# Performance work log

Measured on AMD Instinct MI355X. Metric: run time of the kernel, lower is better.

The kernel has to match this reference:

```python
import jax, jax.numpy as jnp
import numpy as np

PI = 3.1415926
EPS_LN = 1e-5
SLOPE = 0.01  # nn.LeakyReLU default negative_slope


def _leaky(x):
    return jnp.where(x >= 0, x, SLOPE * x)


def _layernorm(x):
    # normalizes over dims (1,2) of [B,C,L], biased variance
    mean = x.mean(axis=(1, 2), keepdims=True)
    var = x.var(axis=(1, 2), keepdims=True)
    return (x - mean) / jnp.sqrt(var + EPS_LN)


def _conv1d(x, w, b):
    # x [B,C,L], w [O,I,3]
    y = jax.lax.conv_general_dilated(x, w, window_strides=(1,), padding='SAME',
                                     dimension_numbers=('NCH', 'OIH', 'NCH'))
    return y + b[None, :, None]


def _conv_stack(x, w1, b1, w2, b2, w3, b3):
    x = _leaky(_layernorm(_conv1d(x, w1, b1)))
    x = _leaky(_layernorm(_conv1d(x, w2, b2)))
    x = _leaky(_layernorm(_conv1d(x, w3, b3)))
    return x


def _context_pooling(feats, w1, b1, w2, b2, w3, b3, r=0.1):
    # feats [B,L,D]
    B, L, D = feats.shape
    sw = _conv_stack(feats.transpose(0, 2, 1), w1, b1, w2, b2, w3, b3)  # [B,2,L]
    s = jax.nn.softmax(sw[:, 0, :], axis=1)  # [B,L]
    w = jax.nn.softmax(sw[:, 1, :], axis=1)  # [B,L]
    std = r * L * s  # [B,L] (per query/center i)
    pos = jnp.arange(L, dtype=feats.dtype)
    diff2 = (pos[None, :] - pos[:, None]) ** 2  # [Li,Lj], (place - center)^2
    g = (2 * PI) ** -0.5 * (std[:, :, None] ** -1) * jnp.exp(
        -diff2[None] / (1e-5 + 2.0 * std[:, :, None] ** 2))  # [B,Li,Lj]
    g = g / jnp.max(g, axis=2, keepdims=True)
    W = g * w[:, None, :]  # [B,Li,Lj]
    return jnp.einsum('bij,bjd->bid', W, feats)


def setup_inputs() -> dict:
    key = jax.random.key(0)
    ks = jax.random.split(key, 16)
    B, L, D = 16, 1024, 640
    D2 = 2 * D
    f32 = jnp.float32
    sc = 0.02
    inp = {
        'feats': jax.random.normal(ks[0], (B, L, D), f32),
        # ContextPooling conv stack
        'cp_w1': jax.random.normal(ks[1], (D2, D, 3), f32) * sc,
        'cp_b1': jnp.zeros((D2,), f32),
        'cp_w2': jax.random.normal(ks[2], (D2, D2, 3), f32) * sc,
        'cp_b2': jnp.zeros((D2,), f32),
        'cp_w3': jax.random.normal(ks[3], (2, D2, 3), f32) * sc,
        'cp_b3': jnp.zeros((2,), f32),
        # SoluModel conv stack
        'cv_w1': jax.random.normal(ks[4], (D2, D, 3), f32) * sc,
        'cv_b1': jnp.zeros((D2,), f32),
        'cv_w2': jax.random.normal(ks[5], (D2, D2, 3), f32) * sc,
        'cv_b2': jnp.zeros((D2,), f32),
        'cv_w3': jax.random.normal(ks[6], (D, D2, 3), f32) * sc,
        'cv_b3': jnp.zeros((D,), f32),
        # MLP: Linear(2D -> D), torch init normal(0, 0.01), bias 0
        'mlp_w': jax.random.normal(ks[7], (D, 2 * D), f32) * 0.01,
        'mlp_b': jnp.zeros((D,), f32),
    }
    return inp


def reference(feats, cp_w1, cp_b1, cp_w2, cp_b2, cp_w3, cp_b3,
              cv_w1, cv_b1, cv_w2, cv_b2, cv_w3, cv_b3, mlp_w, mlp_b):
    out_sa = _context_pooling(feats, cp_w1, cp_b1, cp_w2, cp_b2, cp_w3, cp_b3) + feats
    out_conv = _conv_stack(feats.transpose(0, 2, 1),
                           cv_w1, cv_b1, cv_w2, cv_b2, cv_w3, cv_b3)
    out_conv = out_conv.transpose(0, 2, 1) + feats
    out = jnp.concatenate([out_sa, out_conv], axis=2)  # [B,L,2D]
    # Dropout(p=0.6) is identity at inference
    out = _leaky(jnp.einsum('bld,od->blo', out, mlp_w) + mlp_b)
    return out
```

## Files before the change

kernel.cpp:

```cpp
#include <hip/hip_runtime.h>
#include <hip/hip_bf16.h>
#include <math.h>

#define SLOPE 0.01f
#define EPS_LN 1e-5f

typedef __hip_bfloat16 bf16;
typedef __attribute__((ext_vector_type(8))) short short8;
typedef __attribute__((ext_vector_type(4))) float f32x4;

__device__ __forceinline__ float leakyf(float x) { return x < 0.f ? SLOPE * x : x; }

__device__ __forceinline__ float b2f(short s) {
    unsigned u = ((unsigned)(unsigned short)s) << 16;
    return __builtin_bit_cast(float, u);
}
__device__ __forceinline__ short f2b(float f) {
    __hip_bfloat16 h = __float2bfloat16(f);
    return *(short*)&h;
}

__device__ __forceinline__ void gload_lds16(const void* g, void* l) {
    __builtin_amdgcn_global_load_lds(
        (const __attribute__((address_space(1))) void*)g,
        (__attribute__((address_space(3))) void*)l, 16, 0, 0);
}

template <int EPI>
__global__ __launch_bounds__(256, 2) void gemm_dual(
    const bf16* __restrict__ A0, const bf16* __restrict__ A1, long sA, int ldA,
    const bf16* __restrict__ Bt0, const bf16* __restrict__ Bt1,
    const float* __restrict__ bias0, const float* __restrict__ bias1,
    void* __restrict__ Out0, void* __restrict__ Out1, long sO, int ldO, int K,
    int gx, int gy, int halfwg,
    float2* __restrict__ stats0, float2* __restrict__ stats1)
{
    __shared__ bf16 As[128][64];
    __shared__ bf16 Bs[128][64];

    const int nwg = gridDim.x;
    const int wid = (blockIdx.x & 7) * (nwg >> 3) + (blockIdx.x >> 3);
    const int branch = wid >= halfwg;
    const int w = wid - branch * halfwg;
    const int bx = w % gx;
    const int by = (w / gx) % gy;
    const int bz = w / (gx * gy);

    const bf16* A = branch ? A1 : A0;
    const bf16* Bt = branch ? Bt1 : Bt0;
    const float* bias = branch ? bias1 : bias0;
    void* Outv = branch ? Out1 : Out0;
    float2* stats = branch ? stats1 : stats0;

    const bf16* Ab = A + (long)bz * sA + (long)by * 128 * ldA;
    const bf16* Bb = Bt + (long)bx * 128 * K;
    const int tid = threadIdx.x;
    const int wave = tid >> 6, lane = tid & 63;
    const int moff = (wave >> 1) * 64, noff = (wave & 1) * 64;
    const int r16 = lane & 15, g4 = lane >> 4;
    const int r7 = r16 & 7;

    f32x4 acc[4][4];
#pragma unroll
    for (int i = 0; i < 4; ++i)
#pragma unroll
        for (int j = 0; j < 4; ++j)
            acc[i][j] = (f32x4){0.f, 0.f, 0.f, 0.f};

    for (int k0 = 0; k0 < K; k0 += 64) {
        __syncthreads();
#pragma unroll
        for (int i = 0; i < 4; ++i) {
            int chunk = i * 256 + tid;
            int row = chunk >> 3;
            int kc = (chunk ^ (chunk >> 3)) & 7;
            gload_lds16(Ab + (long)row * ldA + (k0 + kc * 8),
                        (char*)(&As[0][0]) + (i * 256 + wave * 64) * 16);
        }
#pragma unroll
        for (int i = 0; i < 4; ++i) {
            int chunk = i * 256 + tid;
            int row = chunk >> 3;
            int kc = (chunk ^ (chunk >> 3)) & 7;
            gload_lds16(Bb + (long)row * K + (k0 + kc * 8),
                        (char*)(&Bs[0][0]) + (i * 256 + wave * 64) * 16);
        }
        __syncthreads();
#pragma unroll
        for (int kk = 0; kk < 2; ++kk) {
            short8 af[4], bfr[4];
#pragma unroll
            for (int mi = 0; mi < 4; ++mi)
                af[mi] = *(const short8*)&As[moff + mi * 16 + r16][((kk * 4 + g4) ^ r7) * 8];
#pragma unroll
            for (int ni = 0; ni < 4; ++ni)
                bfr[ni] = *(const short8*)&Bs[noff + ni * 16 + r16][((kk * 4 + g4) ^ r7) * 8];
#pragma unroll
            for (int mi = 0; mi < 4; ++mi)
#pragma unroll
                for (int ni = 0; ni < 4; ++ni)
                    acc[mi][ni] = __builtin_amdgcn_mfma_f32_16x16x32_bf16(
                        af[mi], bfr[ni], acc[mi][ni], 0, 0, 0);
        }
    }

    float s = 0.f, q = 0.f;
#pragma unroll
    for (int mi = 0; mi < 4; ++mi) {
#pragma unroll
        for (int ni = 0; ni < 4; ++ni) {
            int col = bx * 128 + noff + ni * 16 + r16;
            float bv = bias[col];
#pragma unroll
            for (int r = 0; r < 4; ++r) {
                int row = by * 128 + moff + mi * 16 + g4 * 4 + r;
                float v = acc[mi][ni][r] + bv;
                if (EPI == 1) {
                    ((float*)Outv)[(long)bz * sO + (long)row * ldO + col] = leakyf(v);
                } else {
                    ((bf16*)Outv)[(long)bz * sO + (long)row * ldO + col] = __float2bfloat16(v);
                    s += v; q += v * v;
                }
            }
        }
    }
    if (EPI == 0) {
        __syncthreads();
        float* red = (float*)&As[0][0];
        float* red2 = red + 256;
        red[tid] = s; red2[tid] = q;
        __syncthreads();
        for (int o = 128; o; o >>= 1) {
            if (tid < o) { red[tid] += red[tid + o]; red2[tid] += red2[tid + o]; }
            __syncthreads();
        }
        if (tid == 0) {
            atomicAdd(&stats[bz].x, red[0]);
            atomicAdd(&stats[bz].y, red2[0]);
        }
    }
}

__device__ __forceinline__ void repack1(const float* __restrict__ w,
                                        bf16* __restrict__ bt, long idx, int CI)
{
    int K3 = 3 * CI;
    int o = (int)(idx / K3);
    int k = (int)(idx % K3);
    int t = k / CI, ci = k % CI;
    bt[idx] = __float2bfloat16(w[(long)o * CI * 3 + ci * 3 + t]);
}

__global__ void prep_k(const float* __restrict__ feats,
                       const float* __restrict__ cp_w1, const float* __restrict__ cv_w1,
                       const float* __restrict__ cp_w2, const float* __restrict__ cv_w2,
                       const float* __restrict__ cp_w3, const float* __restrict__ cv_w3,
                       const float* __restrict__ mlp_w,
                       bf16* __restrict__ xp,
                       bf16* __restrict__ Bm1a, bf16* __restrict__ Bm1b,
                       bf16* __restrict__ Bcp2, bf16* __restrict__ Bcv2,
                       bf16* __restrict__ Bcp3, bf16* __restrict__ Bcv3,
                       bf16* __restrict__ Bmlp, float2* __restrict__ sacc)
{
    long idx = (long)blockIdx.x * 256 + threadIdx.x;
    if (idx < 80) { sacc[idx] = make_float2(0.f, 0.f); return; }
    idx -= 80;
    const long NPACK8 = 16L * 1026 * 640 / 8;
    if (idx < NPACK8) {
        long e = idx * 8;
        int c = (int)(e % 640);
        long t = e / 640;
        int r = (int)(t % 1026);
        int b = (int)(t / 1026);
        short8 o;
        if (r == 0 || r == 1025) {
#pragma unroll
            for (int j = 0; j < 8; ++j) o[j] = 0;
        } else {
            const float* src = feats + ((long)b * 1024 + (r - 1)) * 640 + c;
            f32x4 v0 = *(const f32x4*)src;
            f32x4 v1 = *(const f32x4*)(src + 4);
#pragma unroll
            for (int j = 0; j < 4; ++j) { o[j] = f2b(v0[j]); o[j + 4] = f2b(v1[j]); }
        }
        *(short8*)(xp + e) = o;
        return;
    }
    idx -= NPACK8;
    const long W1 = 1280L * 640 * 3;
    const long W2 = 1280L * 1280 * 3;
    if (idx < W1) { repack1(cp_w1, Bm1a, idx, 640); return; }
    idx -= W1;
    if (idx < W1) { repack1(cv_w1, Bm1b, idx, 640); return; }
    idx -= W1;
    if (idx < W2) { repack1(cp_w2, Bcp2, idx, 1280); return; }
    idx -= W2;
    if (idx < W2) { repack1(cv_w2, Bcv2, idx, 1280); return; }
    idx -= W2;
    if (idx < 2L * 1280 * 3) { repack1(cp_w3, Bcp3, idx, 1280); return; }
    idx -= 2L * 1280 * 3;
    const long W3 = 640L * 1280 * 3;
    if (idx < W3) { repack1(cv_w3, Bcv3, idx, 1280); return; }
    idx -= W3;
    if (idx < 640L * 1280) { Bmlp[idx] = __float2bfloat16(mlp_w[idx]); return; }
}

__global__ void norm_pack2_k(const bf16* __restrict__ y0, const bf16* __restrict__ y1,
                             bf16* __restrict__ x0, bf16* __restrict__ x1,
                             const float2* __restrict__ sacc, int sbase, float invN)
{
    const int prob = blockIdx.y;
    const bf16* y = prob ? y1 : y0;
    bf16* xp = prob ? x1 : x0;
    long i8 = (long)blockIdx.x * 256 + threadIdx.x;
    const long total8 = 16L * 1026 * 1280 / 8;
    if (i8 >= total8) return;
    long e = i8 * 8;
    int c = (int)(e % 1280);
    long t = e / 1280;
    int r = (int)(t % 1026);
    int b = (int)(t / 1026);
    short8 o;
    if (r == 0 || r == 1025) {
#pragma unroll
        for (int j = 0; j < 8; ++j) o[j] = 0;
    } else {
        float2 a = sacc[sbase + prob * 16 + b];
        float m = a.x * invN;
        float rstd = rsqrtf(a.y * invN - m * m + EPS_LN);
        short8 v = *(const short8*)(y + ((long)b * 1024 + (r - 1)) * 1280 + c);
#pragma unroll
        for (int j = 0; j < 8; ++j)
            o[j] = f2b(leakyf((b2f(v[j]) - m) * rstd));
    }
    *(short8*)(xp + e) = o;
}

__global__ void norm_addf_v_k(const bf16* __restrict__ y, const float2* __restrict__ sacc,
                              const float* __restrict__ feats, bf16* __restrict__ acat,
                              float invN)
{
    long i8 = (long)blockIdx.x * 256 + threadIdx.x;
    long total8 = 16L * 1024 * 640 / 8;
    if (i8 >= total8) return;
    long e = i8 * 8;
    int c = (int)(e % 640);
    int l = (int)((e / 640) % 1024);
    int b = (int)(e / (640L * 1024));
    float2 a = sacc[64 + b];
    float m = a.x * invN;
    float rstd = rsqrtf(a.y * invN - m * m + EPS_LN);
    short8 v = *(const short8*)(y + e);
    f32x4 f0 = *(const f32x4*)(feats + e);
    f32x4 f1 = *(const f32x4*)(feats + e + 4);
    short8 o;
#pragma unroll
    for (int j = 0; j < 4; ++j) {
        o[j] = f2b(leakyf((b2f(v[j]) - m) * rstd) + f0[j]);
        o[j + 4] = f2b(leakyf((b2f(v[j + 4]) - m) * rstd) + f1[j]);
    }
    *(short8*)(acat + ((long)b * 1024 + l) * 1280 + 640 + c) = o;
}

__global__ void conv3cp_k(const bf16* __restrict__ xp, const bf16* __restrict__ w3,
                          const float* __restrict__ b3, float* __restrict__ sw)
{
    int wid = (int)((blockIdx.x * 256 + threadIdx.x) >> 6);
    int lane = threadIdx.x & 63;
    int b = wid >> 10, l = wid & 1023;
    const short8* xr = (const short8*)(xp + ((long)b * 1026 + l) * 1280);
    const short8* w0 = (const short8*)w3;
    const short8* w1 = (const short8*)(w3 + 3840);
    float a0 = 0.f, a1 = 0.f;
    for (int c = lane; c < 480; c += 64) {
        short8 x = xr[c], u = w0[c], v = w1[c];
#pragma unroll
        for (int j = 0; j < 8; ++j) {
            float xf = b2f(x[j]);
            a0 += xf * b2f(u[j]);
            a1 += xf * b2f(v[j]);
        }
    }
    for (int o = 32; o; o >>= 1) { a0 += __shfl_down(a0, o); a1 += __shfl_down(a1, o); }
    if (lane == 0) {
        sw[b * 2048 + l] = a0 + b3[0];
        sw[b * 2048 + 1024 + l] = a1 + b3[1];
    }
}

__global__ __launch_bounds__(256) void cp_post_k(const float* __restrict__ sw,
                                                 float* __restrict__ stdb,
                                                 float* __restrict__ wb)
{
    int b = blockIdx.x, tid = threadIdx.x;
    __shared__ float s0[1024], s1[1024], red[256];
    const float* p = sw + b * 2048;
    float s = 0.f, q = 0.f;
    for (int l = tid; l < 1024; l += 256) {
        float v0 = p[l], v1 = p[1024 + l];
        s0[l] = v0; s1[l] = v1;
        s += v0 + v1; q += v0 * v0 + v1 * v1;
    }
    red[tid] = s; __syncthreads();
    for (int o = 128; o; o >>= 1) { if (tid < o) red[tid] += red[tid + o]; __syncthreads(); }
    float mean = red[0] / 2048.f; __syncthreads();
    red[tid] = q; __syncthreads();
    for (int o = 128; o; o >>= 1) { if (tid < o) red[tid] += red[tid + o]; __syncthreads(); }
    float inv = rsqrtf(red[0] / 2048.f - mean * mean + EPS_LN); __syncthreads();
    for (int l = tid; l < 1024; l += 256) {
        s0[l] = leakyf((s0[l] - mean) * inv);
        s1[l] = leakyf((s1[l] - mean) * inv);
    }
    __syncthreads();
    float mx = -1e30f;
    for (int l = tid; l < 1024; l += 256) mx = fmaxf(mx, s0[l]);
    red[tid] = mx; __syncthreads();
    for (int o = 128; o; o >>= 1) { if (tid < o) red[tid] = fmaxf(red[tid], red[tid + o]); __syncthreads(); }
    mx = red[0]; __syncthreads();
    float se = 0.f;
    for (int l = tid; l < 1024; l += 256) { float e = __expf(s0[l] - mx); s0[l] = e; se += e; }
    red[tid] = se; __syncthreads();
    for (int o = 128; o; o >>= 1) { if (tid < o) red[tid] += red[tid + o]; __syncthreads(); }
    float rs = 1.f / red[0]; __syncthreads();
    for (int l = tid; l < 1024; l += 256) stdb[b * 1024 + l] = 102.4f * s0[l] * rs;
    mx = -1e30f;
    for (int l = tid; l < 1024; l += 256) mx = fmaxf(mx, s1[l]);
    red[tid] = mx; __syncthreads();
    for (int o = 128; o; o >>= 1) { if (tid < o) red[tid] = fmaxf(red[tid], red[tid + o]); __syncthreads(); }
    mx = red[0]; __syncthreads();
    se = 0.f;
    for (int l = tid; l < 1024; l += 256) { float e = __expf(s1[l] - mx); s1[l] = e; se += e; }
    red[tid] = se; __syncthreads();
    for (int o = 128; o; o >>= 1) { if (tid < o) red[tid] += red[tid + o]; __syncthreads(); }
    rs = 1.f / red[0]; __syncthreads();
    for (int l = tid; l < 1024; l += 256) wb[b * 1024 + l] = s1[l] * rs;
}

__global__ __launch_bounds__(256) void pool_k(const float* __restrict__ feats,
                                              const float* __restrict__ stdb,
                                              const float* __restrict__ wb,
                                              bf16* __restrict__ acat)
{
    int i = blockIdx.x, b = blockIdx.y, tid = threadIdx.x;
    float sd = stdb[b * 1024 + i];
    float den = 1e-5f + 2.f * sd * sd;
    float inv = 1.f / den;
    int R = (int)sqrtf(11.5129255f * den) + 1;
    int jlo = max(0, i - R), jhi = min(1023, i + R);
    __shared__ float cj[256];
    float a0 = 0.f, a1 = 0.f, a2 = 0.f;
    const float* fb = feats + (long)b * 1024 * 640;
    for (int j0 = jlo; j0 <= jhi; j0 += 256) {
        int j = j0 + tid;
        float c = 0.f;
        if (j <= jhi) {
            float d = (float)(j - i);
            c = __expf(-d * d * inv) * wb[b * 1024 + j];
        }
        __syncthreads();
        cj[tid] = c;
        __syncthreads();
        int lim = min(256, jhi - j0 + 1);
        for (int t = 0; t < lim; ++t) {
            float cc = cj[t];
            const float* fr = fb + (long)(j0 + t) * 640;
            a0 += cc * fr[tid];
            a1 += cc * fr[tid + 256];
            if (tid < 128) a2 += cc * fr[tid + 512];
        }
    }
    long obase = ((long)b * 1024 + i) * 1280;
    long fbase = ((long)b * 1024 + i) * 640;
    acat[obase + tid] = __float2bfloat16(a0 + feats[fbase + tid]);
    acat[obase + tid + 256] = __float2bfloat16(a1 + feats[fbase + tid + 256]);
    if (tid < 128) acat[obase + tid + 512] = __float2bfloat16(a2 + feats[fbase + tid + 512]);
}

extern "C" void kernel_launch(void* const* d_in, const int* in_sizes, int n_in,
                              void* d_out, int out_size, void* d_ws, size_t ws_size,
                              hipStream_t stream)
{
    const float* feats = (const float*)d_in[0];
    const float* cp_w1 = (const float*)d_in[1];
    const float* cp_b1 = (const float*)d_in[2];
    const float* cp_w2 = (const float*)d_in[3];
    const float* cp_b2 = (const float*)d_in[4];
    const float* cp_w3 = (const float*)d_in[5];
    const float* cp_b3 = (const float*)d_in[6];
    const float* cv_w1 = (const float*)d_in[7];
    const float* cv_b1 = (const float*)d_in[8];
    const float* cv_w2 = (const float*)d_in[9];
    const float* cv_b2 = (const float*)d_in[10];
    const float* cv_w3 = (const float*)d_in[11];
    const float* cv_b3 = (const float*)d_in[12];
    const float* mlp_w = (const float*)d_in[13];
    const float* mlp_b = (const float*)d_in[14];
    float* out = (float*)d_out;

    char* ws = (char*)d_ws;
    size_t off = 0;
    auto alloc = [&](size_t bytes) -> char* {
        char* p = ws + off;
        off += (bytes + 255) & ~(size_t)255;
        return p;
    };
    char* R1 = alloc(16L * 1024 * 1280 * 2);
    bf16* XpadF = (bf16*)R1;
    bf16* Acat = (bf16*)R1;
    bf16* Xp_cp = (bf16*)alloc(16L * 1026 * 1280 * 2);
    bf16* Xp_cv = (bf16*)alloc(16L * 1026 * 1280 * 2);
    bf16* Y0 = (bf16*)alloc(16L * 1024 * 1280 * 2);
    bf16* Y1 = (bf16*)alloc(16L * 1024 * 1280 * 2);
    bf16* Ycv3 = Y0;
    bf16* Bm1 = (bf16*)alloc(2560L * 1920 * 2);
    bf16* Bcp2 = (bf16*)alloc(1280L * 3840 * 2);
    bf16* Bcv2 = (bf16*)alloc(1280L * 3840 * 2);
    bf16* Bcp3 = (bf16*)alloc(2L * 3840 * 2);
    bf16* Bcv3 = (bf16*)alloc(640L * 3840 * 2);
    bf16* Bmlp = (bf16*)alloc(640L * 1280 * 2);
    float* swb = (float*)alloc(16L * 2048 * 4);
    float* stdb = (float*)alloc(16L * 1024 * 4);
    float* wbf = (float*)alloc(16L * 1024 * 4);
    float2* sacc = (float2*)alloc(80L * 8);
    (void)ws_size; (void)in_sizes; (void)n_in; (void)out_size;

    const long N28 = 16L * 1026 * 1280 / 8;
    const long NA8 = 16L * 1024 * 640 / 8;
    const long N1280 = 1024L * 1280, N640 = 1024L * 640;
    const float inv1280 = 1.f / (float)N1280, inv640 = 1.f / (float)N640;

    const long NPREP = 80 + 16L * 1026 * 640 / 8 + 2 * (1280L * 640 * 3)
                     + 2 * (1280L * 1280 * 3) + 2L * 1280 * 3
                     + 640L * 1280 * 3 + 640L * 1280;
    prep_k<<<(int)((NPREP + 255) / 256), 256, 0, stream>>>(
        feats, cp_w1, cv_w1, cp_w2, cv_w2, cp_w3, cv_w3, mlp_w,
        XpadF, Bm1, Bm1 + 1280L * 1920, Bcp2, Bcv2, Bcp3, Bcv3, Bmlp, sacc);

    gemm_dual<0><<<2560, 256, 0, stream>>>(
        XpadF, XpadF, 1026L * 640, 640, Bm1, Bm1 + 1280L * 1920,
        cp_b1, cv_b1, Y0, Y1, N1280, 1280, 1920, 10, 8, 1280,
        sacc, sacc + 16);
    norm_pack2_k<<<dim3((N28 + 255) / 256, 2), 256, 0, stream>>>(
        Y0, Y1, Xp_cp, Xp_cv, sacc, 0, inv1280);

    gemm_dual<0><<<2560, 256, 0, stream>>>(
        Xp_cp, Xp_cv, 1026L * 1280, 1280, Bcp2, Bcv2,
        cp_b2, cv_b2, Y0, Y1, N1280, 1280, 3840, 10, 8, 1280,
        sacc + 32, sacc + 48);
    norm_pack2_k<<<dim3((N28 + 255) / 256, 2), 256, 0, stream>>>(
        Y0, Y1, Xp_cp, Xp_cv, sacc, 32, inv1280);

    conv3cp_k<<<4096, 256, 0, stream>>>(Xp_cp, Bcp3, cp_b3, swb);
    cp_post_k<<<16, 256, 0, stream>>>(swb, stdb, wbf);
    pool_k<<<dim3(1024, 16), 256, 0, stream>>>(feats, stdb, wbf, Acat);

    gemm_dual<0><<<640, 256, 0, stream>>>(
        Xp_cv, Xp_cv, 1026L * 1280, 1280, Bcv3, Bcv3,
        cv_b3, cv_b3, Ycv3, Ycv3, N640, 640, 3840, 5, 8, 640,
        sacc + 64, sacc + 64);
    norm_addf_v_k<<<(NA8 + 255) / 256, 256, 0, stream>>>(Ycv3, sacc, feats, Acat, inv640);

    gemm_dual<1><<<640, 256, 0, stream>>>(
        Acat, Acat, N1280, 1280, Bmlp, Bmlp,
        mlp_b, mlp_b, out, out, N640, 640, 1280, 5, 8, 640,
        nullptr, nullptr);
}
```

Measured before the change: 738.1 us.

## Fuse cv3 GEMM and context pooling into one heterogeneous launch with 4-query pool blocks

```diff
diff --git a/kernel.cpp b/kernel.cpp
--- a/kernel.cpp
+++ b/kernel.cpp
@@ -137,6 +137,158 @@
         if (tid == 0) {
             atomicAdd(&stats[bz].x, red[0]);
             atomicAdd(&stats[bz].y, red2[0]);
+        }
+    }
+}
+
+__global__ __launch_bounds__(256, 2) void cv3_pool_k(
+    const bf16* __restrict__ Axp, const bf16* __restrict__ Bt,
+    const float* __restrict__ bias, bf16* __restrict__ Y,
+    float2* __restrict__ stats,
+    const float* __restrict__ feats, const float* __restrict__ stdb,
+    const float* __restrict__ wb, bf16* __restrict__ acat)
+{
+    __shared__ bf16 As[128][64];
+    __shared__ bf16 Bs[128][64];
+    __shared__ float cj4[4][256];
+
+    const int tid = threadIdx.x;
+    if (blockIdx.x < 640) {
+        const int wid = (blockIdx.x & 7) * 80 + (blockIdx.x >> 3);
+        const int bx = wid % 5;
+        const int by = (wid / 5) % 8;
+        const int bz = wid / 40;
+        const int K = 3840;
+        const bf16* Ab = Axp + ((long)bz * 1026 + (long)by * 128) * 1280;
+        const bf16* Bb = Bt + (long)bx * 128 * K;
+        const int wave = tid >> 6, lane = tid & 63;
+        const int moff = (wave >> 1) * 64, noff = (wave & 1) * 64;
+        const int r16 = lane & 15, g4 = lane >> 4;
+        const int r7 = r16 & 7;
+
+        f32x4 acc[4][4];
+#pragma unroll
+        for (int i = 0; i < 4; ++i)
+#pragma unroll
+            for (int j = 0; j < 4; ++j)
+                acc[i][j] = (f32x4){0.f, 0.f, 0.f, 0.f};
+
+        for (int k0 = 0; k0 < K; k0 += 64) {
+            __syncthreads();
+#pragma unroll
+            for (int i = 0; i < 4; ++i) {
+                int chunk = i * 256 + tid;
+                int row = chunk >> 3;
+                int kc = (chunk ^ (chunk >> 3)) & 7;
+                gload_lds16(Ab + (long)row * 1280 + (k0 + kc * 8),
+                            (char*)(&As[0][0]) + (i * 256 + wave * 64) * 16);
+            }
+#pragma unroll
+            for (int i = 0; i < 4; ++i) {
+                int chunk = i * 256 + tid;
+                int row = chunk >> 3;
+                int kc = (chunk ^ (chunk >> 3)) & 7;
+                gload_lds16(Bb + (long)row * K + (k0 + kc * 8),
+                            (char*)(&Bs[0][0]) + (i * 256 + wave * 64) * 16);
+            }
+            __syncthreads();
+#pragma unroll
+            for (int kk = 0; kk < 2; ++kk) {
+                short8 af[4], bfr[4];
+#pragma unroll
+                for (int mi = 0; mi < 4; ++mi)
+                    af[mi] = *(const short8*)&As[moff + mi * 16 + r16][((kk * 4 + g4) ^ r7) * 8];
+#pragma unroll
+                for (int ni = 0; ni < 4; ++ni)
+                    bfr[ni] = *(const short8*)&Bs[noff + ni * 16 + r16][((kk * 4 + g4) ^ r7) * 8];
+#pragma unroll
+                for (int mi = 0; mi < 4; ++mi)
+#pragma unroll
+                    for (int ni = 0; ni < 4; ++ni)
+                        acc[mi][ni] = __builtin_amdgcn_mfma_f32_16x16x32_bf16(
+                            af[mi], bfr[ni], acc[mi][ni], 0, 0, 0);
+            }
+        }
+
+        float s = 0.f, q = 0.f;
+#pragma unroll
+        for (int mi = 0; mi < 4; ++mi) {
+#pragma unroll
+            for (int ni = 0; ni < 4; ++ni) {
+                int col = bx * 128 + noff + ni * 16 + r16;
+                float bv = bias[col];
+#pragma unroll
+                for (int r = 0; r < 4; ++r) {
+                    int row = by * 128 + moff + mi * 16 + g4 * 4 + r;
+                    float v = acc[mi][ni][r] + bv;
+                    Y[((long)bz * 1024 + row) * 640 + col] = __float2bfloat16(v);
+                    s += v; q += v * v;
+                }
+            }
+        }
+        __syncthreads();
+        float* red = (float*)&As[0][0];
+        float* red2 = red + 256;
+        red[tid] = s; red2[tid] = q;
+        __syncthreads();
+        for (int o = 128; o; o >>= 1) {
+            if (tid < o) { red[tid] += red[tid + o]; red2[tid] += red2[tid + o]; }
+            __syncthreads();
+        }
+        if (tid == 0) {
+            atomicAdd(&stats[bz].x, red[0]);
+            atomicAdd(&stats[bz].y, red2[0]);
+        }
+    } else {
+        const int pw = blockIdx.x - 640;
+        const int b = pw >> 8;
+        const int i0 = (pw & 255) * 4;
+        float invq[4];
+        int jloU = 1024, jhiU = -1;
+#pragma unroll
+        for (int q = 0; q < 4; ++q) {
+            float sd = stdb[b * 1024 + i0 + q];
+            float den = 1e-5f + 2.f * sd * sd;
+            invq[q] = 1.f / den;
+            int R = (int)sqrtf(11.5129255f * den) + 1;
+            int jl = max(0, i0 + q - R), jh = min(1023, i0 + q + R);
+            jloU = min(jloU, jl); jhiU = max(jhiU, jh);
+        }
+        float a[4][3];
+#pragma unroll
+        for (int q = 0; q < 4; ++q) { a[q][0] = 0.f; a[q][1] = 0.f; a[q][2] = 0.f; }
+        const float* fb = feats + (long)b * 1024 * 640;
+        for (int j0 = jloU; j0 <= jhiU; j0 += 256) {
+            int j = j0 + tid;
+            float wj = (j <= jhiU) ? wb[b * 1024 + j] : 0.f;
+            __syncthreads();
+#pragma unroll
+            for (int q = 0; q < 4; ++q) {
+                float d = (float)(j - (i0 + q));
+                cj4[q][tid] = __expf(-d * d * invq[q]) * wj;
+            }
+            __syncthreads();
+            int lim = min(256, jhiU - j0 + 1);
+            for (int t = 0; t < lim; ++t) {
+                const float* fr = fb + (long)(j0 + t) * 640;
+                float f0 = fr[tid];
+                float f1 = fr[tid + 256];
+                float f2 = (tid < 128) ? fr[tid + 512] : 0.f;
+#pragma unroll
+                for (int q = 0; q < 4; ++q) {
+                    float cc = cj4[q][t];
+                    a[q][0] += cc * f0; a[q][1] += cc * f1; a[q][2] += cc * f2;
+                }
+            }
+        }
+#pragma unroll
+        for (int q = 0; q < 4; ++q) {
+            long obase = ((long)b * 1024 + i0 + q) * 1280;
+            long fbase = ((long)b * 1024 + i0 + q) * 640;
+            acat[obase + tid] = __float2bfloat16(a[q][0] + feats[fbase + tid]);
+            acat[obase + tid + 256] = __float2bfloat16(a[q][1] + feats[fbase + tid + 256]);
+            if (tid < 128)
+                acat[obase + tid + 512] = __float2bfloat16(a[q][2] + feats[fbase + tid + 512]);
         }
     }
 }
@@ -334,46 +486,6 @@
     for (int o = 128; o; o >>= 1) { if (tid < o) red[tid] += red[tid + o]; __syncthreads(); }
     rs = 1.f / red[0]; __syncthreads();
     for (int l = tid; l < 1024; l += 256) wb[b * 1024 + l] = s1[l] * rs;
-}
-
-__global__ __launch_bounds__(256) void pool_k(const float* __restrict__ feats,
-                                              const float* __restrict__ stdb,
-                                              const float* __restrict__ wb,
-                                              bf16* __restrict__ acat)
-{
-    int i = blockIdx.x, b = blockIdx.y, tid = threadIdx.x;
-    float sd = stdb[b * 1024 + i];
-    float den = 1e-5f + 2.f * sd * sd;
-    float inv = 1.f / den;
-    int R = (int)sqrtf(11.5129255f * den) + 1;
-    int jlo = max(0, i - R), jhi = min(1023, i + R);
-    __shared__ float cj[256];
-    float a0 = 0.f, a1 = 0.f, a2 = 0.f;
-    const float* fb = feats + (long)b * 1024 * 640;
-    for (int j0 = jlo; j0 <= jhi; j0 += 256) {
-        int j = j0 + tid;
-        float c = 0.f;
-        if (j <= jhi) {
-            float d = (float)(j - i);
-            c = __expf(-d * d * inv) * wb[b * 1024 + j];
-        }
-        __syncthreads();
-        cj[tid] = c;
-        __syncthreads();
-        int lim = min(256, jhi - j0 + 1);
-        for (int t = 0; t < lim; ++t) {
-            float cc = cj[t];
-            const float* fr = fb + (long)(j0 + t) * 640;
-            a0 += cc * fr[tid];
-            a1 += cc * fr[tid + 256];
-            if (tid < 128) a2 += cc * fr[tid + 512];
-        }
-    }
-    long obase = ((long)b * 1024 + i) * 1280;
-    long fbase = ((long)b * 1024 + i) * 640;
-    acat[obase + tid] = __float2bfloat16(a0 + feats[fbase + tid]);
-    acat[obase + tid + 256] = __float2bfloat16(a1 + feats[fbase + tid + 256]);
-    if (tid < 128) acat[obase + tid + 512] = __float2bfloat16(a2 + feats[fbase + tid + 512]);
 }
 
 extern "C" void kernel_launch(void* const* d_in, const int* in_sizes, int n_in,
@@ -452,12 +564,10 @@
 
     conv3cp_k<<<4096, 256, 0, stream>>>(Xp_cp, Bcp3, cp_b3, swb);
     cp_post_k<<<16, 256, 0, stream>>>(swb, stdb, wbf);
-    pool_k<<<dim3(1024, 16), 256, 0, stream>>>(feats, stdb, wbf, Acat);
-
-    gemm_dual<0><<<640, 256, 0, stream>>>(
-        Xp_cv, Xp_cv, 1026L * 1280, 1280, Bcv3, Bcv3,
-        cv_b3, cv_b3, Ycv3, Ycv3, N640, 640, 3840, 5, 8, 640,
-        sacc + 64, sacc + 64);
+
+    cv3_pool_k<<<640 + 4096, 256, 0, stream>>>(
+        Xp_cv, Bcv3, cv_b3, Ycv3, sacc + 64,
+        feats, stdb, wbf, Acat);
     norm_addf_v_k<<<(NA8 + 255) / 256, 256, 0, stream>>>(Ycv3, sacc, feats, Acat, inv640);
 
     gemm_dual<1><<<640, 256, 0, stream>>>(
```

New measurement: 720.9 us. 2.3% less time.
